# Optimization experiments

Measured on AMD Instinct MI355X. Metric: run time of the kernel, lower is better.

## Reference

```python
import jax, jax.numpy as jnp
import numpy as np

B, S, D, F, E = 4, 2048, 1024, 4096, 8


def setup_inputs() -> dict:
    key = jax.random.key(0)
    ks = jax.random.split(key, 7)
    s1 = 1.0 / np.sqrt(D)
    s2 = 1.0 / np.sqrt(F)
    x = jax.random.normal(ks[0], (B, S, D), dtype=jnp.float32)
    # Stacked expert weights: linear1 (D->F), linear2 (F->D), torch default uniform init
    W1 = jax.random.uniform(ks[1], (E, D, F), jnp.float32, -s1, s1)
    b1 = jax.random.uniform(ks[2], (E, F), jnp.float32, -s1, s1)
    W2 = jax.random.uniform(ks[3], (E, F, D), jnp.float32, -s2, s2)
    b2 = jax.random.uniform(ks[4], (E, D), jnp.float32, -s2, s2)
    Wr = jax.random.uniform(ks[5], (D, E), jnp.float32, -s1, s1)
    br = jax.random.uniform(ks[6], (E,), jnp.float32, -s1, s1)
    return {"x": x, "W1": W1, "b1": b1, "W2": W2, "b2": b2, "Wr": Wr, "br": br}


def reference(x, W1, b1, W2, b2, Wr, br):
    b, s, d = x.shape
    e = Wr.shape[1]
    logits = x @ Wr + br                      # [B,S,E]
    idx = jnp.argmax(logits, axis=-1)         # top-1 expert per token
    probs = jax.nn.softmax(logits, axis=-1)
    gates = jnp.take_along_axis(probs, idx[..., None], axis=-1)[..., 0]  # [B,S]
    xf = x.reshape(-1, d)                     # [N,D]
    idxf = idx.reshape(-1)
    gf = gates.reshape(-1)
    out = jnp.zeros_like(xf)
    for ei in range(e):                       # fixed small expert count
        h = jax.nn.gelu(xf @ W1[ei] + b1[ei], approximate=False)  # exact gelu like F.gelu
        y = h @ W2[ei] + b2[ei]
        mask = (idxf == ei).astype(xf.dtype)
        out = out + y * (gf * mask)[:, None]
    return out.reshape(b, s, d)
```

## Files before the change

kernel.cpp:

```cpp
#include <hip/hip_runtime.h>
#include <stdint.h>
#include <math.h>

#define NTOK 8192
#define DIM  1024
#define FDIM 4096
#define NEXP 8

typedef __bf16 bf16x8 __attribute__((ext_vector_type(8)));
typedef float floatx4 __attribute__((ext_vector_type(4)));
typedef unsigned int u32;

__device__ __forceinline__ unsigned short f2b(float f) {
  union { float f; unsigned u; } v; v.f = f;
  return (unsigned short)((v.u + 0x7fffu + ((v.u >> 16) & 1u)) >> 16);
}

__device__ __forceinline__ float gelu_f(float x) {
  float u = 1.5957691216f * x * (1.0f + 0.044715f * x * x);
  return x / (1.0f + __expf(-u));
}

__device__ __forceinline__ void async_cp16(const unsigned short* g, unsigned short* l) {
  __builtin_amdgcn_global_load_lds((__attribute__((address_space(1))) u32*)g,
                                   (__attribute__((address_space(3))) u32*)l, 16, 0, 0);
}

__device__ __forceinline__ void expert_tile(const int* __restrict__ ctrl, int mt,
                                            int& e, int& m0, int& cnt, int& ntiles) {
  int off = 0, ts = 0;
  e = 0; m0 = 0; cnt = 0;
#pragma unroll
  for (int i = 0; i < NEXP; i++) {
    int c = ctrl[i];
    int nt = (c + 127) >> 7;
    if (mt >= ts && mt < ts + nt) {
      e = i;
      m0 = off + (mt - ts) * 128;
      cnt = c - (mt - ts) * 128;
    }
    ts += nt; off += c;
  }
  ntiles = ts;
  if (cnt > 128) cnt = 128;
}

__global__ __launch_bounds__(256) void router_cvt_k(
    const float* __restrict__ x, const float* __restrict__ Wr,
    const float* __restrict__ br, int* __restrict__ idx,
    float* __restrict__ gate, int* __restrict__ ctrl,
    unsigned short* __restrict__ Xc) {
  int t = (int)((blockIdx.x * 256 + threadIdx.x) >> 6);
  int lane = threadIdx.x & 63;
  const float* xr = x + (size_t)t * DIM;
  unsigned short* xo = Xc + (size_t)t * DIM;
  float acc[NEXP];
#pragma unroll
  for (int e = 0; e < NEXP; e++) acc[e] = 0.f;
#pragma unroll
  for (int k = 0; k < DIM / 64; k++) {
    int d = k * 64 + lane;
    float xv = xr[d];
    xo[d] = f2b(xv);
    const float4* wp = (const float4*)(Wr + (size_t)d * NEXP);
    float4 w0 = wp[0], w1 = wp[1];
    acc[0] += xv * w0.x; acc[1] += xv * w0.y;
    acc[2] += xv * w0.z; acc[3] += xv * w0.w;
    acc[4] += xv * w1.x; acc[5] += xv * w1.y;
    acc[6] += xv * w1.z; acc[7] += xv * w1.w;
  }
#pragma unroll
  for (int off = 32; off > 0; off >>= 1) {
#pragma unroll
    for (int e = 0; e < NEXP; e++) acc[e] += __shfl_xor(acc[e], off, 64);
  }
  if (lane == 0) {
    float mx = -3.4e38f; int best = 0;
#pragma unroll
    for (int e = 0; e < NEXP; e++) {
      float l = acc[e] + br[e];
      if (l > mx) { mx = l; best = e; }
    }
    float s = 0.f;
#pragma unroll
    for (int e = 0; e < NEXP; e++) s += expf(acc[e] + br[e] - mx);
    idx[t] = best;
    gate[t] = 1.f / s;
    atomicAdd(&ctrl[best], 1);
  }
}

__global__ __launch_bounds__(256) void perm_k(
    const int* __restrict__ idx, const float* __restrict__ gate,
    int* __restrict__ ctrl, int* __restrict__ perm, float* __restrict__ gate_p) {
  int t = blockIdx.x * 256 + threadIdx.x;
  int e = idx[t];
  int off = 0;
#pragma unroll
  for (int i = 0; i < NEXP; i++) off += (i < e) ? ctrl[i] : 0;
  int pos = off + atomicAdd(&ctrl[17 + e], 1);
  perm[pos] = t;
  gate_p[pos] = gate[t];
}

__global__ __launch_bounds__(256) void transpose_cvt2_k(
    const float* __restrict__ W1, unsigned short* __restrict__ W1b,
    const float* __restrict__ W2, unsigned short* __restrict__ W2b) {
  __shared__ float tile[64][65];
  __shared__ unsigned short obuf[64][72];
  int z = blockIdx.z;
  const float* in; unsigned short* out; int R, C, tc, tr;
  if (z < NEXP) {
    in = W1 + (size_t)z * DIM * FDIM; out = W1b + (size_t)z * DIM * FDIM;
    R = DIM; C = FDIM; tc = blockIdx.x; tr = blockIdx.y;
  } else {
    int e = z - NEXP;
    in = W2 + (size_t)e * FDIM * DIM; out = W2b + (size_t)e * FDIM * DIM;
    R = FDIM; C = DIM; tc = blockIdx.y; tr = blockIdx.x;
  }
  int c0 = tc * 64, r0 = tr * 64;
  int t = threadIdx.x;
  int rr = t >> 4, cc = (t & 15) * 4;
#pragma unroll
  for (int k = 0; k < 64; k += 16) {
    float4 v = *(const float4*)&in[(size_t)(r0 + rr + k) * C + c0 + cc];
    tile[rr + k][cc] = v.x; tile[rr + k][cc + 1] = v.y;
    tile[rr + k][cc + 2] = v.z; tile[rr + k][cc + 3] = v.w;
  }
  __syncthreads();
  int cr = t >> 4, rb = (t & 15) * 4;
#pragma unroll
  for (int k = 0; k < 64; k += 16) {
    ushort4 o;
    o.x = f2b(tile[rb + 0][cr + k]); o.y = f2b(tile[rb + 1][cr + k]);
    o.z = f2b(tile[rb + 2][cr + k]); o.w = f2b(tile[rb + 3][cr + k]);
    *(ushort4*)&obuf[cr + k][rb] = o;
  }
  __syncthreads();
  int r2 = t >> 3, c8 = (t & 7) * 8;
#pragma unroll
  for (int k = 0; k < 64; k += 32)
    *(uint4*)&out[(size_t)(c0 + r2 + k) * R + r0 + c8] = *(const uint4*)&obuf[r2 + k][c8];
}

__global__ __launch_bounds__(256) void gemm1_k(
    const unsigned short* __restrict__ Xc, const unsigned short* __restrict__ Bmat,
    const float* __restrict__ bias, unsigned short* __restrict__ Hout,
    const int* __restrict__ ctrl, const int* __restrict__ perm) {
  __shared__ unsigned short lds[16384];
  unsigned short* A_lds = lds;
  unsigned short* B_lds = lds + 8192;

  int mt = blockIdx.y;
  int e, m0, cnt, ntiles;
  expert_tile(ctrl, mt, e, m0, cnt, ntiles);
  if (mt >= ntiles) return;
  int c0 = blockIdx.x * 128;
  const unsigned short* B = Bmat + (size_t)e * FDIM * DIM;

  int tid = threadIdx.x;
  int lane = tid & 63, wave = tid >> 6;
  int wr = wave >> 1, wc = wave & 1;
  int grp = lane >> 4, m16 = lane & 15;

  int lr = lane >> 3;
  int cchunk = (lane & 7) ^ lr;
  const unsigned short* srcA[4];
  const unsigned short* srcB[4];
  unsigned short* dstA[4];
  unsigned short* dstB[4];
#pragma unroll
  for (int q = 0; q < 4; q++) {
    int brow = wave * 32 + q * 8;
    int p = m0 + brow + lr; if (p > NTOK - 1) p = NTOK - 1;
    int arow = perm[p];
    srcA[q] = Xc + (size_t)arow * DIM + cchunk * 8;
    srcB[q] = B + (size_t)(c0 + brow + lr) * DIM + cchunk * 8;
    dstA[q] = A_lds + brow * 64;
    dstB[q] = B_lds + brow * 64;
  }

  floatx4 acc[4][4];
  floatx4 zero = {0.f, 0.f, 0.f, 0.f};
#pragma unroll
  for (int i = 0; i < 4; i++)
#pragma unroll
    for (int j = 0; j < 4; j++) acc[i][j] = zero;

  int x7 = m16 & 7;
  int rowA[4], rowB[4];
#pragma unroll
  for (int i = 0; i < 4; i++) {
    rowA[i] = (wr * 64 + i * 16 + m16) * 64;
    rowB[i] = (wc * 64 + i * 16 + m16) * 64;
  }

  for (int kk = 0; kk < DIM; kk += 64) {
#pragma unroll
    for (int q = 0; q < 4; q++) async_cp16(srcA[q], dstA[q]);
#pragma unroll
    for (int q = 0; q < 4; q++) async_cp16(srcB[q], dstB[q]);
#pragma unroll
    for (int q = 0; q < 4; q++) { srcA[q] += 64; srcB[q] += 64; }
    __syncthreads();
    bf16x8 af[2][4], bfr[2][4];
#pragma unroll
    for (int h = 0; h < 2; h++) {
      int off = (((h << 2) | grp) ^ x7) << 3;
#pragma unroll
      for (int i = 0; i < 4; i++) {
        af[h][i]  = *(const bf16x8*)&A_lds[rowA[i] + off];
        bfr[h][i] = *(const bf16x8*)&B_lds[rowB[i] + off];
      }
    }
#pragma unroll
    for (int h = 0; h < 2; h++)
#pragma unroll
      for (int i = 0; i < 4; i++)
#pragma unroll
        for (int j = 0; j < 4; j++)
          acc[i][j] = __builtin_amdgcn_mfma_f32_16x16x32_bf16(af[h][i], bfr[h][j], acc[i][j], 0, 0, 0);
    __syncthreads();
  }

  float bs[4];
#pragma unroll
  for (int j = 0; j < 4; j++) bs[j] = bias[(size_t)e * FDIM + c0 + wc * 64 + j * 16 + m16];

  unsigned short* st = lds + wave * 4096;
#pragma unroll
  for (int i = 0; i < 4; i++)
#pragma unroll
    for (int j = 0; j < 4; j++)
#pragma unroll
      for (int r = 0; r < 4; r++) {
        int row = i * 16 + grp * 4 + r;
        int scol = (j * 16 + m16) ^ (((row >> 1) & 7) << 3);
        st[row * 64 + scol] = f2b(gelu_f(acc[i][j][r] + bs[j]));
      }
  __syncthreads();
  int lr8 = lane >> 3, c8 = (lane & 7) * 8;
  int colb = c0 + wc * 64 + c8;
#pragma unroll
  for (int rr = 0; rr < 8; rr++) {
    int row = rr * 8 + lr8;
    int gm = wr * 64 + row;
    if (gm < cnt) {
      int scol = c8 ^ (((row >> 1) & 7) << 3);
      *(uint4*)&Hout[(size_t)(m0 + gm) * FDIM + colb] = *(const uint4*)&st[row * 64 + scol];
    }
  }
}

__global__ __launch_bounds__(256) void gemm2_k(
    const unsigned short* __restrict__ Hmat, const unsigned short* __restrict__ W2b,
    const float* __restrict__ b2, float* __restrict__ out,
    const int* __restrict__ perm, const float* __restrict__ gate_p,
    const int* __restrict__ ctrl) {
  __shared__ unsigned short lds[32768];

  int mt = blockIdx.y;
  int e, m0, cnt, ntiles;
  expert_tile(ctrl, mt, e, m0, cnt, ntiles);
  if (mt >= ntiles) return;
  int c0 = blockIdx.x * 128;
  const unsigned short* B = W2b + (size_t)e * DIM * FDIM;

  int tid = threadIdx.x;
  int lane = tid & 63, wave = tid >> 6;
  int wr = wave >> 1, wc = wave & 1;
  int grp = lane >> 4, m16 = lane & 15;

  int lr = lane >> 3;
  int cchunk = (lane & 7) ^ lr;
  const unsigned short* srcA[4];
  const unsigned short* srcB[4];
  int dstoff[4];
#pragma unroll
  for (int q = 0; q < 4; q++) {
    int brow = wave * 32 + q * 8;
    int arow = m0 + brow + lr; if (arow > NTOK - 1) arow = NTOK - 1;
    srcA[q] = Hmat + (size_t)arow * FDIM + cchunk * 8;
    srcB[q] = B + (size_t)(c0 + brow + lr) * FDIM + cchunk * 8;
    dstoff[q] = brow * 64;
  }

  floatx4 acc[4][4];
  floatx4 zero = {0.f, 0.f, 0.f, 0.f};
#pragma unroll
  for (int i = 0; i < 4; i++)
#pragma unroll
    for (int j = 0; j < 4; j++) acc[i][j] = zero;

  int x7 = m16 & 7;
  int rowA[4], rowB[4];
#pragma unroll
  for (int i = 0; i < 4; i++) {
    rowA[i] = (wr * 64 + i * 16 + m16) * 64;
    rowB[i] = (wc * 64 + i * 16 + m16) * 64;
  }

#pragma unroll
  for (int q = 0; q < 4; q++) async_cp16(srcA[q], lds + dstoff[q]);
#pragma unroll
  for (int q = 0; q < 4; q++) async_cp16(srcB[q], lds + 8192 + dstoff[q]);
#pragma unroll
  for (int q = 0; q < 4; q++) { srcA[q] += 64; srcB[q] += 64; }

  const int kIters = FDIM / 64;
  int p = 0;
  for (int it = 0; it < kIters; ++it) {
    __syncthreads();
    unsigned short* Acur = lds + p * 16384;
    unsigned short* Bcur = Acur + 8192;
    if (it + 1 < kIters) {
      unsigned short* An = lds + (p ^ 1) * 16384;
      unsigned short* Bn = An + 8192;
#pragma unroll
      for (int q = 0; q < 4; q++) async_cp16(srcA[q], An + dstoff[q]);
#pragma unroll
      for (int q = 0; q < 4; q++) async_cp16(srcB[q], Bn + dstoff[q]);
#pragma unroll
      for (int q = 0; q < 4; q++) { srcA[q] += 64; srcB[q] += 64; }
    }
    bf16x8 af[2][4], bfr[2][4];
#pragma unroll
    for (int h = 0; h < 2; h++) {
      int off = (((h << 2) | grp) ^ x7) << 3;
#pragma unroll
      for (int i = 0; i < 4; i++) {
        af[h][i]  = *(const bf16x8*)&Acur[rowA[i] + off];
        bfr[h][i] = *(const bf16x8*)&Bcur[rowB[i] + off];
      }
    }
#pragma unroll
    for (int h = 0; h < 2; h++)
#pragma unroll
      for (int i = 0; i < 4; i++)
#pragma unroll
        for (int j = 0; j < 4; j++)
          acc[i][j] = __builtin_amdgcn_mfma_f32_16x16x32_bf16(af[h][i], bfr[h][j], acc[i][j], 0, 0, 0);
    p ^= 1;
  }

  float bs[4];
#pragma unroll
  for (int j = 0; j < 4; j++) bs[j] = b2[(size_t)e * DIM + c0 + wc * 64 + j * 16 + m16];

#pragma unroll
  for (int i = 0; i < 4; i++) {
    int rb = wr * 64 + i * 16 + grp * 4;
#pragma unroll
    for (int r = 0; r < 4; r++) {
      int lm = rb + r;
      if (lm < cnt) {
        int t = perm[m0 + lm];
        float g = gate_p[m0 + lm];
#pragma unroll
        for (int j = 0; j < 4; j++) {
          int col = c0 + wc * 64 + j * 16 + m16;
          out[(size_t)t * DIM + col] = (acc[i][j][r] + bs[j]) * g;
        }
      }
    }
  }
}

extern "C" void kernel_launch(void* const* d_in, const int* in_sizes, int n_in,
                              void* d_out, int out_size, void* d_ws, size_t ws_size,
                              hipStream_t stream) {
  const float* x  = (const float*)d_in[0];
  const float* W1 = (const float*)d_in[1];
  const float* b1 = (const float*)d_in[2];
  const float* W2 = (const float*)d_in[3];
  const float* b2 = (const float*)d_in[4];
  const float* Wr = (const float*)d_in[5];
  const float* br = (const float*)d_in[6];
  float* out = (float*)d_out;

  char* w = (char*)d_ws;
  int*   ctrl   = (int*)w;
  int*   idx    = (int*)(w + 1024);
  float* gate   = (float*)(w + 1024 + 4 * NTOK);
  int*   perm   = (int*)(w + 1024 + 8 * NTOK);
  float* gate_p = (float*)(w + 1024 + 12 * NTOK);
  unsigned short* Xc  = (unsigned short*)(w + (1ull << 18));
  unsigned short* H   = (unsigned short*)(w + (20ull << 20));
  unsigned short* W1b = (unsigned short*)(w + (88ull << 20));
  unsigned short* W2b = (unsigned short*)(w + (156ull << 20));

  hipMemsetAsync(ctrl, 0, 256, stream);
  transpose_cvt2_k<<<dim3(64, 16, 16), 256, 0, stream>>>(W1, W1b, W2, W2b);
  router_cvt_k<<<NTOK / 4, 256, 0, stream>>>(x, Wr, br, idx, gate, ctrl, Xc);
  perm_k<<<NTOK / 256, 256, 0, stream>>>(idx, gate, ctrl, perm, gate_p);
  gemm1_k<<<dim3(FDIM / 128, 72), 256, 0, stream>>>(Xc, W1b, b1, H, ctrl, perm);
  gemm2_k<<<dim3(DIM / 128, 72), 256, 0, stream>>>(H, W2b, b2, out, perm, gate_p, ctrl);
}
```

Baseline: 714.8 us.

## Double-buffer gemm1 K-loop, aggregate perm atomics per wave, simplify weight transpose

The gemm1 main loop now uses two LDS buffers with a K step of 32, prefetching the next tile while MFMAs run on the current one and dropping the second barrier per iteration. perm_k replaces per-thread atomics with one wave-level ballot and atomic per expert. The weight transpose kernel converts to bf16 before writing to LDS, removing the fp32 tile and one sync. The gemm change risks a missing wait on the async LDS loads before compute, and halving K per iteration doubles the number of barriers.

```diff
diff --git a/kernel.cpp b/kernel.cpp
--- a/kernel.cpp
+++ b/kernel.cpp
@@ -94,11 +94,24 @@
     const int* __restrict__ idx, const float* __restrict__ gate,
     int* __restrict__ ctrl, int* __restrict__ perm, float* __restrict__ gate_p) {
   int t = blockIdx.x * 256 + threadIdx.x;
+  int lane = threadIdx.x & 63;
   int e = idx[t];
   int off = 0;
 #pragma unroll
   for (int i = 0; i < NEXP; i++) off += (i < e) ? ctrl[i] : 0;
-  int pos = off + atomicAdd(&ctrl[17 + e], 1);
+  int pos = 0;
+#pragma unroll
+  for (int ei = 0; ei < NEXP; ei++) {
+    unsigned long long m = __ballot(e == ei);
+    if (m) {
+      int leader = (int)__ffsll((long long)m) - 1;
+      int base = 0;
+      if (lane == leader) base = atomicAdd(&ctrl[17 + ei], (int)__popcll(m));
+      base = __shfl(base, leader, 64);
+      if (e == ei)
+        pos = off + base + (int)__popcll(m & ((1ull << lane) - 1ull));
+    }
+  }
   perm[pos] = t;
   gate_p[pos] = gate[t];
 }
@@ -106,8 +119,7 @@
 __global__ __launch_bounds__(256) void transpose_cvt2_k(
     const float* __restrict__ W1, unsigned short* __restrict__ W1b,
     const float* __restrict__ W2, unsigned short* __restrict__ W2b) {
-  __shared__ float tile[64][65];
-  __shared__ unsigned short obuf[64][72];
+  __shared__ unsigned short obuf[64][68];
   int z = blockIdx.z;
   const float* in; unsigned short* out; int R, C, tc, tr;
   if (z < NEXP) {
@@ -120,27 +132,32 @@
   }
   int c0 = tc * 64, r0 = tr * 64;
   int t = threadIdx.x;
-  int rr = t >> 4, cc = (t & 15) * 4;
-#pragma unroll
-  for (int k = 0; k < 64; k += 16) {
-    float4 v = *(const float4*)&in[(size_t)(r0 + rr + k) * C + c0 + cc];
-    tile[rr + k][cc] = v.x; tile[rr + k][cc + 1] = v.y;
-    tile[rr + k][cc + 2] = v.z; tile[rr + k][cc + 3] = v.w;
+  int rr2 = t >> 4;
+  int cc = (t & 15) * 4;
+#pragma unroll
+  for (int k = 0; k < 2; k++) {
+    int rb = rr2 * 2 + 32 * k;
+    float4 v0 = *(const float4*)&in[(size_t)(r0 + rb) * C + c0 + cc];
+    float4 v1 = *(const float4*)&in[(size_t)(r0 + rb + 1) * C + c0 + cc];
+    u32 w0 = (u32)f2b(v0.x) | ((u32)f2b(v1.x) << 16);
+    u32 w1 = (u32)f2b(v0.y) | ((u32)f2b(v1.y) << 16);
+    u32 w2 = (u32)f2b(v0.z) | ((u32)f2b(v1.z) << 16);
+    u32 w3 = (u32)f2b(v0.w) | ((u32)f2b(v1.w) << 16);
+    *(u32*)&obuf[cc + 0][rb] = w0;
+    *(u32*)&obuf[cc + 1][rb] = w1;
+    *(u32*)&obuf[cc + 2][rb] = w2;
+    *(u32*)&obuf[cc + 3][rb] = w3;
   }
   __syncthreads();
-  int cr = t >> 4, rb = (t & 15) * 4;
-#pragma unroll
-  for (int k = 0; k < 64; k += 16) {
-    ushort4 o;
-    o.x = f2b(tile[rb + 0][cr + k]); o.y = f2b(tile[rb + 1][cr + k]);
-    o.z = f2b(tile[rb + 2][cr + k]); o.w = f2b(tile[rb + 3][cr + k]);
-    *(ushort4*)&obuf[cr + k][rb] = o;
-  }
-  __syncthreads();
-  int r2 = t >> 3, c8 = (t & 7) * 8;
-#pragma unroll
-  for (int k = 0; k < 64; k += 32)
-    *(uint4*)&out[(size_t)(c0 + r2 + k) * R + r0 + c8] = *(const uint4*)&obuf[r2 + k][c8];
+  int c8 = (t & 7) * 8, r2 = t >> 3;
+#pragma unroll
+  for (int k = 0; k < 2; k++) {
+    int Rr = r2 + 32 * k;
+    uint2 a = *(const uint2*)&obuf[Rr][c8];
+    uint2 b = *(const uint2*)&obuf[Rr][c8 + 4];
+    uint4 v; v.x = a.x; v.y = a.y; v.z = b.x; v.w = b.y;
+    *(uint4*)&out[(size_t)(c0 + Rr) * R + r0 + c8] = v;
+  }
 }
 
 __global__ __launch_bounds__(256) void gemm1_k(
@@ -148,8 +165,6 @@
     const float* __restrict__ bias, unsigned short* __restrict__ Hout,
     const int* __restrict__ ctrl, const int* __restrict__ perm) {
   __shared__ unsigned short lds[16384];
-  unsigned short* A_lds = lds;
-  unsigned short* B_lds = lds + 8192;
 
   int mt = blockIdx.y;
   int e, m0, cnt, ntiles;
@@ -163,21 +178,19 @@
   int wr = wave >> 1, wc = wave & 1;
   int grp = lane >> 4, m16 = lane & 15;
 
-  int lr = lane >> 3;
-  int cchunk = (lane & 7) ^ lr;
-  const unsigned short* srcA[4];
-  const unsigned short* srcB[4];
-  unsigned short* dstA[4];
-  unsigned short* dstB[4];
-#pragma unroll
-  for (int q = 0; q < 4; q++) {
-    int brow = wave * 32 + q * 8;
-    int p = m0 + brow + lr; if (p > NTOK - 1) p = NTOK - 1;
+  int lr4 = lane >> 2;
+  int kc = (lane & 3) ^ (lr4 & 3);
+  const unsigned short* srcA[2];
+  const unsigned short* srcB[2];
+  int dstoff[2];
+#pragma unroll
+  for (int q = 0; q < 2; q++) {
+    int brow = wave * 32 + q * 16 + lr4;
+    int p = m0 + brow; if (p > NTOK - 1) p = NTOK - 1;
     int arow = perm[p];
-    srcA[q] = Xc + (size_t)arow * DIM + cchunk * 8;
-    srcB[q] = B + (size_t)(c0 + brow + lr) * DIM + cchunk * 8;
-    dstA[q] = A_lds + brow * 64;
-    dstB[q] = B_lds + brow * 64;
+    srcA[q] = Xc + (size_t)arow * DIM + kc * 8;
+    srcB[q] = B + (size_t)(c0 + brow) * DIM + kc * 8;
+    dstoff[q] = (wave * 32 + q * 16) * 32;
   }
 
   floatx4 acc[4][4];
@@ -187,41 +200,49 @@
 #pragma unroll
     for (int j = 0; j < 4; j++) acc[i][j] = zero;
 
-  int x7 = m16 & 7;
   int rowA[4], rowB[4];
 #pragma unroll
   for (int i = 0; i < 4; i++) {
-    rowA[i] = (wr * 64 + i * 16 + m16) * 64;
-    rowB[i] = (wc * 64 + i * 16 + m16) * 64;
-  }
-
-  for (int kk = 0; kk < DIM; kk += 64) {
-#pragma unroll
-    for (int q = 0; q < 4; q++) async_cp16(srcA[q], dstA[q]);
-#pragma unroll
-    for (int q = 0; q < 4; q++) async_cp16(srcB[q], dstB[q]);
-#pragma unroll
-    for (int q = 0; q < 4; q++) { srcA[q] += 64; srcB[q] += 64; }
+    rowA[i] = (wr * 64 + i * 16 + m16) * 32;
+    rowB[i] = (wc * 64 + i * 16 + m16) * 32;
+  }
+  int roff = (grp ^ (m16 & 3)) * 8;
+
+#pragma unroll
+  for (int q = 0; q < 2; q++) async_cp16(srcA[q], lds + dstoff[q]);
+#pragma unroll
+  for (int q = 0; q < 2; q++) async_cp16(srcB[q], lds + 4096 + dstoff[q]);
+#pragma unroll
+  for (int q = 0; q < 2; q++) { srcA[q] += 32; srcB[q] += 32; }
+
+  const int kIters = DIM / 32;
+  int p = 0;
+  for (int it = 0; it < kIters; ++it) {
     __syncthreads();
-    bf16x8 af[2][4], bfr[2][4];
-#pragma unroll
-    for (int h = 0; h < 2; h++) {
-      int off = (((h << 2) | grp) ^ x7) << 3;
-#pragma unroll
-      for (int i = 0; i < 4; i++) {
-        af[h][i]  = *(const bf16x8*)&A_lds[rowA[i] + off];
-        bfr[h][i] = *(const bf16x8*)&B_lds[rowB[i] + off];
-      }
-    }
-#pragma unroll
-    for (int h = 0; h < 2; h++)
-#pragma unroll
-      for (int i = 0; i < 4; i++)
-#pragma unroll
-        for (int j = 0; j < 4; j++)
-          acc[i][j] = __builtin_amdgcn_mfma_f32_16x16x32_bf16(af[h][i], bfr[h][j], acc[i][j], 0, 0, 0);
-    __syncthreads();
-  }
+    unsigned short* Acur = lds + p * 8192;
+    unsigned short* Bcur = Acur + 4096;
+    if (it + 1 < kIters) {
+      unsigned short* An = lds + (p ^ 1) * 8192;
+#pragma unroll
+      for (int q = 0; q < 2; q++) async_cp16(srcA[q], An + dstoff[q]);
+#pragma unroll
+      for (int q = 0; q < 2; q++) async_cp16(srcB[q], An + 4096 + dstoff[q]);
+#pragma unroll
+      for (int q = 0; q < 2; q++) { srcA[q] += 32; srcB[q] += 32; }
+    }
+    bf16x8 af[4], bfr[4];
+#pragma unroll
+    for (int i = 0; i < 4; i++) af[i] = *(const bf16x8*)&Acur[rowA[i] + roff];
+#pragma unroll
+    for (int j = 0; j < 4; j++) bfr[j] = *(const bf16x8*)&Bcur[rowB[j] + roff];
+#pragma unroll
+    for (int i = 0; i < 4; i++)
+#pragma unroll
+      for (int j = 0; j < 4; j++)
+        acc[i][j] = __builtin_amdgcn_mfma_f32_16x16x32_bf16(af[i], bfr[j], acc[i][j], 0, 0, 0);
+    p ^= 1;
+  }
+  __syncthreads();
 
   float bs[4];
 #pragma unroll
```

New measurement: 679.8 us. 1.05x faster.
